# Kernel tuning notes

Hardware: AMD Instinct MI355X
Metric: run time of the kernel (lower is better)

The kernel has to match this reference:

```python
import jax, jax.numpy as jnp
import numpy as np

HEADS = 8

def _conv1x1(x, W, b):
    # x: [n, Cin, H, W]; W: [Cout, Cin]; b: [Cout]
    return jnp.einsum('nchw,oc->nohw', x, W) + b[None, :, None, None]

def setup_inputs() -> dict:
    key = jax.random.key(0)
    ks = jax.random.split(key, 11)
    n, Cin, H, W = 8, 256, 80, 80
    Ck, Cv = 256, 256
    s_in = 1.0 / np.sqrt(Cin)
    s_v = 1.0 / np.sqrt(Cv)
    return {
        'query_feature': jax.random.normal(ks[0], (n, Cin, H, W), jnp.float32),
        'key_feature': jax.random.normal(ks[1], (n, Cin, H, W), jnp.float32),
        'value_feature': jax.random.normal(ks[2], (n, Cin, H, W), jnp.float32),
        'Wq': jax.random.normal(ks[3], (Ck, Cin), jnp.float32) * s_in,
        'bq': jax.random.normal(ks[4], (Ck,), jnp.float32) * s_in,
        'Wk': jax.random.normal(ks[5], (Ck, Cin), jnp.float32) * s_in,
        'bk': jax.random.normal(ks[6], (Ck,), jnp.float32) * s_in,
        'Wv': jax.random.normal(ks[7], (Cv, Cin), jnp.float32) * s_in,
        'bv': jax.random.normal(ks[8], (Cv,), jnp.float32) * s_in,
        'Wr': jax.random.normal(ks[9], (Cin, Cv), jnp.float32) * s_v,
        'br': jax.random.normal(ks[10], (Cin,), jnp.float32) * s_v,
    }

def reference(query_feature, key_feature, value_feature, Wq, bq, Wk, bk, Wv, bv, Wr, br):
    n, _, qh, qw = query_feature.shape
    kvn, _, kvh, kvw = key_feature.shape
    Ck = Wq.shape[0]
    Cv = Wv.shape[0]
    hk = Ck // HEADS
    hv = Cv // HEADS
    Lq = qh * qw
    Lkv = kvh * kvw
    # 1x1 conv projections, split channels into heads (consecutive channel blocks)
    q = _conv1x1(query_feature, Wq, bq).reshape(n, HEADS, hk, Lq)
    k = _conv1x1(key_feature, Wk, bk).reshape(kvn, HEADS, hk, Lkv)
    v = _conv1x1(value_feature, Wv, bv).reshape(kvn, HEADS, hv, Lkv)
    # softmax: keys over spatial positions, queries over head channels
    k = jax.nn.softmax(k, axis=3)
    q = jax.nn.softmax(q, axis=2)
    # efficient (linear) attention: context = K @ V^T, out = context^T @ Q
    context = jnp.einsum('nhkl,nhvl->nhkv', k, v)          # [n, H, hk, hv]
    attended = jnp.einsum('nhkv,nhkl->nhvl', context, q)   # [n, H, hv, Lq]
    aggregated = attended.reshape(n, Cv, qh, qw)
    return _conv1x1(aggregated, Wr, br) + query_feature
```

## Files before the change

### kernel.cpp

```cpp
#include <hip/hip_runtime.h>
#include <hip/hip_bf16.h>

#define NB 8
#define C 256
#define LL 6400
#define HEADS 8
#define HC 32
#define NH 64
#define SEG 40
#define SL 160
#define ATP 40
#define QPP 264

typedef unsigned short u16;
typedef unsigned int u32;
typedef __attribute__((ext_vector_type(8))) short bf16x8;
typedef __attribute__((ext_vector_type(4))) float f32x4;

typedef __attribute__((address_space(1))) const u32 ga_u32;
typedef __attribute__((address_space(3))) u32 ls_u32;

__device__ __forceinline__ void gload_lds16(const u16* g, u16* l) {
  __builtin_amdgcn_global_load_lds((ga_u32*)g, (ls_u32*)l, 16, 0, 0);
}

__device__ __forceinline__ float bf2f(u32 u) { return __uint_as_float(u << 16); }
__device__ __forceinline__ u16 f2bf(float f) {
  __hip_bfloat16 h = __float2bfloat16(f);
  return *(u16*)&h;
}
__device__ __forceinline__ void unpack8(uint4 u, float* f) {
  f[0] = bf2f(u.x & 0xffffu); f[1] = bf2f(u.x >> 16);
  f[2] = bf2f(u.y & 0xffffu); f[3] = bf2f(u.y >> 16);
  f[4] = bf2f(u.z & 0xffffu); f[5] = bf2f(u.z >> 16);
  f[6] = bf2f(u.w & 0xffffu); f[7] = bf2f(u.w >> 16);
}

struct WcvtArgs { const float* W[3]; u16* Wb[3]; };
struct PFArgs { const float* X[3]; const u16* Wb[3]; const float* bias[3]; u16* P[3]; };

__global__ __launch_bounds__(256) void wcvt(WcvtArgs a) {
  const int idx = blockIdx.x * 256 + threadIdx.x;
  const int which = idx >> 14, off = (idx & 16383) * 4;
  float4 v = *(const float4*)&a.W[which][off];
  ushort4 o = {f2bf(v.x), f2bf(v.y), f2bf(v.z), f2bf(v.w)};
  *(ushort4*)&a.Wb[which][off] = o;
}

__global__ __launch_bounds__(256, 2) void proj_fused(PFArgs args) {
  __shared__ __align__(16) u16 At[128 * ATP];
  __shared__ __align__(16) u16 Bs[256 * 32];
  const int which = blockIdx.y >> 3, n = blockIdx.y & 7;
  const int l0 = blockIdx.x * 128;
  const int t = threadIdx.x;
  const int lane = t & 63, wave = t >> 6;
  const int fr = lane & 15, q = lane >> 4;
  const int wl = (wave >> 1) * 64, wco = (wave & 1) * 128;
  const int s32 = t & 31, rcg = t >> 5;
  const int srow = t >> 2, scol = (t & 3) * 8;
  const float* X = args.X[which] + (size_t)n * C * LL;
  const u16* Wb = args.Wb[which];
  f32x4 acc[4][8] = {};
  float4 xv[4];
#pragma unroll
  for (int j = 0; j < 4; ++j)
    xv[j] = *(const float4*)&X[(size_t)(rcg * 4 + j) * LL + l0 + s32 * 4];
  for (int k0 = 0; k0 < C; k0 += 32) {
    __syncthreads();
#pragma unroll
    for (int s = 0; s < 4; ++s)
      gload_lds16(&Wb[(size_t)(s * 64 + srow) * C + k0 + scol],
                  &Bs[s * 2048 + wave * 512]);
    const float* xf = (const float*)xv;
#pragma unroll
    for (int li = 0; li < 4; ++li) {
      const int lp = li ^ (s32 & 3);
      u32 lo = (u32)f2bf(xf[0 * 4 + lp]) | ((u32)f2bf(xf[1 * 4 + lp]) << 16);
      u32 hi = (u32)f2bf(xf[2 * 4 + lp]) | ((u32)f2bf(xf[3 * 4 + lp]) << 16);
      u32* dst = (u32*)&At[(s32 * 4 + lp) * ATP + rcg * 4];
      dst[0] = lo; dst[1] = hi;
    }
    __syncthreads();
    if (k0 + 32 < C) {
#pragma unroll
      for (int j = 0; j < 4; ++j)
        xv[j] = *(const float4*)&X[(size_t)(k0 + 32 + rcg * 4 + j) * LL + l0 + s32 * 4];
    }
    bf16x8 a[4];
#pragma unroll
    for (int i = 0; i < 4; ++i)
      a[i] = *(const bf16x8*)&At[(wl + i * 16 + fr) * ATP + q * 8];
#pragma unroll
    for (int j = 0; j < 8; ++j) {
      bf16x8 b = *(const bf16x8*)&Bs[(wco + j * 16 + fr) * 32 + q * 8];
#pragma unroll
      for (int i = 0; i < 4; ++i)
        acc[i][j] = __builtin_amdgcn_mfma_f32_16x16x32_bf16(a[i], b, acc[i][j], 0, 0, 0);
    }
  }
  const float* bias = args.bias[which];
  u16* P = args.P[which] + (size_t)n * LL * C;
  float bb[8];
#pragma unroll
  for (int j = 0; j < 8; ++j) bb[j] = bias[wco + j * 16 + fr];
#pragma unroll
  for (int i = 0; i < 4; ++i)
#pragma unroll
    for (int r = 0; r < 4; ++r) {
      const int lrow = l0 + wl + i * 16 + q * 4 + r;
#pragma unroll
      for (int j = 0; j < 8; ++j)
        P[(size_t)lrow * C + wco + j * 16 + fr] = f2bf(acc[i][j][r] + bb[j]);
    }
}

__global__ __launch_bounds__(256) void ctx_part(const u16* __restrict__ Kt,
    const u16* __restrict__ Vt, float* __restrict__ pctx, float* __restrict__ psum) {
  __shared__ __align__(16) u16 Ks[16 * 256];
  __shared__ __align__(16) u16 Vs[16 * 256];
  const int seg = blockIdx.x, n = blockIdx.y;
  const int t = threadIdx.x, lane = t & 63, wave = t >> 6;
  const int l0 = seg * SL;
  const u16* KtN = Kt + (size_t)n * LL * C;
  const u16* VtN = Vt + (size_t)n * LL * C;
  const int k4 = (lane & 7) * 4, v8 = lane >> 3;
  float acc[2][4][4] = {};
  float ssum[2][4] = {};
  for (int ls = 0; ls < SL; ls += 16) {
    __syncthreads();
#pragma unroll
    for (int i = 0; i < 2; ++i) {
      const int r = wave * 4 + i * 2;
      gload_lds16(&KtN[(size_t)(l0 + ls + r) * C + lane * 8], &Ks[r * 256]);
      gload_lds16(&VtN[(size_t)(l0 + ls + r) * C + lane * 8], &Vs[r * 256]);
    }
    __syncthreads();
#pragma unroll
    for (int hh = 0; hh < 2; ++hh) {
      const int h = wave * 2 + hh;
#pragma unroll
      for (int l = 0; l < 16; ++l) {
        ushort4 ku = *(const ushort4*)&Ks[l * 256 + h * 32 + k4];
        ushort4 vu = *(const ushort4*)&Vs[l * 256 + h * 32 + v8 * 4];
        float ek[4] = {__expf(bf2f(ku.x)), __expf(bf2f(ku.y)),
                       __expf(bf2f(ku.z)), __expf(bf2f(ku.w))};
        float vf[4] = {bf2f(vu.x), bf2f(vu.y), bf2f(vu.z), bf2f(vu.w)};
#pragma unroll
        for (int i = 0; i < 4; ++i)
#pragma unroll
          for (int j = 0; j < 4; ++j) acc[hh][i][j] = fmaf(ek[i], vf[j], acc[hh][i][j]);
        if (v8 == 0)
#pragma unroll
          for (int i = 0; i < 4; ++i) ssum[hh][i] += ek[i];
      }
    }
  }
#pragma unroll
  for (int hh = 0; hh < 2; ++hh) {
    const int h = wave * 2 + hh;
    const size_t pb = ((size_t)seg * NH + n * 8 + h) * 1024;
#pragma unroll
    for (int i = 0; i < 4; ++i)
#pragma unroll
      for (int j = 0; j < 4; ++j)
        pctx[pb + (size_t)(k4 + i) * 32 + v8 * 4 + j] = acc[hh][i][j];
    if (v8 == 0) {
      const size_t sb = ((size_t)seg * NH + n * 8 + h) * 32;
#pragma unroll
      for (int i = 0; i < 4; ++i) psum[sb + k4 + i] = ssum[hh][i];
    }
  }
}

__global__ __launch_bounds__(256) void ctx_reduce(const float* __restrict__ pctx,
    const float* __restrict__ psum, float* __restrict__ ctx) {
  const int idx = blockIdx.x * 256 + threadIdx.x;
  const int nh = idx >> 10, e = idx & 1023, k = e >> 5;
  float s = 0.f, ss = 0.f;
  for (int g = 0; g < SEG; ++g) {
    s += pctx[(size_t)(g * NH + nh) * 1024 + e];
    ss += psum[(size_t)(g * NH + nh) * 32 + k];
  }
  ctx[idx] = s / ss;
}

__global__ __launch_bounds__(256) void mfuse(const float* __restrict__ Wr,
    const float* __restrict__ ctx, u16* __restrict__ M) {
  const int idx = blockIdx.x * 256 + threadIdx.x;
  const int hk = idx & 255;
  const int o = (idx >> 8) & 255;
  const int n = idx >> 16;
  const int h = hk >> 5, k = hk & 31;
  const float* wr = Wr + (size_t)o * C + h * HC;
  const float* cx = ctx + ((size_t)(n * HEADS + h) * HC + k) * HC;
  float s = 0.f;
#pragma unroll
  for (int v = 0; v < HC; ++v) s = fmaf(wr[v], cx[v], s);
  M[idx] = f2bf(s);
}

__global__ __launch_bounds__(256) void out_fused(const u16* __restrict__ Qt,
    const u16* __restrict__ Mb, const float* __restrict__ br,
    const float* __restrict__ Xq, float* __restrict__ out) {
  __shared__ __align__(16) u16 Qp[64 * QPP];
  __shared__ __align__(16) u16 As[128 * 32];
  const int n = blockIdx.y, l0 = blockIdx.x * 64;
  const int t = threadIdx.x, lane = t & 63, wave = t >> 6;
  const int fr = lane & 15, q = lane >> 4;
  const int wcoL = (wave >> 1) * 64, wl = (wave & 1) * 32;
  const u16* QtN = Qt + (size_t)n * LL * C;
#pragma unroll
  for (int p = 0; p < 2; ++p) {
    const int row = p * 32 + (t >> 3);
    const int g = t & 7;
    const uint4* src = (const uint4*)&QtN[(size_t)(l0 + row) * C + g * 32];
    uint4 u0 = src[0], u1 = src[1], u2 = src[2], u3 = src[3];
    float v[32];
    unpack8(u0, v); unpack8(u1, v + 8); unpack8(u2, v + 16); unpack8(u3, v + 24);
    float e[32], s = 0.f;
#pragma unroll
    for (int j = 0; j < 32; ++j) { e[j] = __expf(v[j]); s += e[j]; }
    const float r = 1.0f / s;
    uint4* drow = (uint4*)&Qp[row * QPP + g * 32];
#pragma unroll
    for (int b4 = 0; b4 < 4; ++b4) {
      union { uint4 u; u16 h[8]; } o;
#pragma unroll
      for (int j = 0; j < 8; ++j) o.h[j] = f2bf(e[b4 * 8 + j] * r);
      drow[b4] = o.u;
    }
  }
  f32x4 acc[2][4][2] = {};
  const u16* MbN = Mb + (size_t)n * C * C;
  const int srow = t >> 2, scol = (t & 3) * 8;
  for (int coh = 0; coh < 2; ++coh)
    for (int k0 = 0; k0 < C; k0 += 32) {
      __syncthreads();
#pragma unroll
      for (int s = 0; s < 2; ++s)
        gload_lds16(&MbN[(size_t)(coh * 128 + s * 64 + srow) * C + k0 + scol],
                    &As[s * 2048 + wave * 512]);
      __syncthreads();
      bf16x8 a[4], b[2];
#pragma unroll
      for (int i = 0; i < 4; ++i)
        a[i] = *(const bf16x8*)&As[(wcoL + i * 16 + fr) * 32 + q * 8];
#pragma unroll
      for (int j = 0; j < 2; ++j)
        b[j] = *(const bf16x8*)&Qp[(wl + j * 16 + fr) * QPP + k0 + q * 8];
#pragma unroll
      for (int i = 0; i < 4; ++i)
#pragma unroll
        for (int j = 0; j < 2; ++j)
          acc[coh][i][j] = __builtin_amdgcn_mfma_f32_16x16x32_bf16(a[i], b[j], acc[coh][i][j], 0, 0, 0);
    }
  const float* XqN = Xq + (size_t)n * C * LL;
  float* On = out + (size_t)n * C * LL;
#pragma unroll
  for (int coh = 0; coh < 2; ++coh)
#pragma unroll
    for (int i = 0; i < 4; ++i)
#pragma unroll
      for (int r = 0; r < 4; ++r) {
        const int co = coh * 128 + wcoL + i * 16 + q * 4 + r;
        const float bb = br[co];
#pragma unroll
        for (int j = 0; j < 2; ++j) {
          const int l = l0 + wl + j * 16 + fr;
          const size_t off = (size_t)co * LL + l;
          On[off] = acc[coh][i][j][r] + bb + XqN[off];
        }
      }
}

extern "C" void kernel_launch(void* const* d_in, const int* in_sizes, int n_in,
                              void* d_out, int out_size, void* d_ws, size_t ws_size,
                              hipStream_t stream) {
  const float* Xq = (const float*)d_in[0];
  const float* Xk = (const float*)d_in[1];
  const float* Xv = (const float*)d_in[2];
  const float* Wq = (const float*)d_in[3];
  const float* bq = (const float*)d_in[4];
  const float* Wk = (const float*)d_in[5];
  const float* bk = (const float*)d_in[6];
  const float* Wv = (const float*)d_in[7];
  const float* bv = (const float*)d_in[8];
  const float* Wr = (const float*)d_in[9];
  const float* br = (const float*)d_in[10];
  float* out = (float*)d_out;

  char* ws = (char*)d_ws;
  const size_t nelem = (size_t)NB * LL * C;
  u16* Qt = (u16*)ws;
  u16* Kt = (u16*)(ws + nelem * 2);
  u16* Vt = (u16*)(ws + nelem * 4);
  char* p = ws + nelem * 6;
  u16* Wqb = (u16*)p; p += C * C * 2;
  u16* Wkb = (u16*)p; p += C * C * 2;
  u16* Wvb = (u16*)p; p += C * C * 2;
  float* pctx = (float*)p; p += (size_t)SEG * NH * HC * HC * 4;
  float* psum = (float*)p; p += (size_t)SEG * NH * HC * 4;
  float* ctx = (float*)p;  p += (size_t)NH * HC * HC * 4;
  u16* Mb = (u16*)p;

  WcvtArgs wa;
  wa.W[0] = Wq; wa.W[1] = Wk; wa.W[2] = Wv;
  wa.Wb[0] = Wqb; wa.Wb[1] = Wkb; wa.Wb[2] = Wvb;
  wcvt<<<192, 256, 0, stream>>>(wa);

  PFArgs pa;
  pa.X[0] = Xq; pa.X[1] = Xk; pa.X[2] = Xv;
  pa.Wb[0] = Wqb; pa.Wb[1] = Wkb; pa.Wb[2] = Wvb;
  pa.bias[0] = bq; pa.bias[1] = bk; pa.bias[2] = bv;
  pa.P[0] = Qt; pa.P[1] = Kt; pa.P[2] = Vt;
  proj_fused<<<dim3(50, 24), 256, 0, stream>>>(pa);

  ctx_part<<<dim3(SEG, NB), 256, 0, stream>>>(Kt, Vt, pctx, psum);
  ctx_reduce<<<NH * HC * HC / 256, 256, 0, stream>>>(pctx, psum, ctx);
  mfuse<<<NB * C * C / 256, 256, 0, stream>>>(Wr, ctx, Mb);
  out_fused<<<dim3(100, NB), 256, 0, stream>>>(Qt, Mb, br, Xq, out);
}
```

Baseline: 347.5 us.

## Double-buffer LDS tiles in projection and output GEMM kernels

Converts the K-loops of proj_fused and out_fused to use double-buffered LDS tiles. The next tile's weight/M loads and X conversion are issued before the current tile's MFMAs, with one barrier per iteration instead of two and explicit waitcnt/sched_barrier control. This is meant to overlap global-to-LDS transfers with compute. In exchange it doubles LDS use, which may reduce occupancy, and relies on hand-tuned vmcnt counts that must match the number of outstanding loads.

```diff
diff --git a/kernel.cpp b/kernel.cpp
--- a/kernel.cpp
+++ b/kernel.cpp
@@ -48,8 +48,8 @@
 }
 
 __global__ __launch_bounds__(256, 2) void proj_fused(PFArgs args) {
-  __shared__ __align__(16) u16 At[128 * ATP];
-  __shared__ __align__(16) u16 Bs[256 * 32];
+  __shared__ __align__(16) u16 At[2][128 * ATP];
+  __shared__ __align__(16) u16 Bs[2][256 * 32];
   const int which = blockIdx.y >> 3, n = blockIdx.y & 7;
   const int l0 = blockIdx.x * 128;
   const int t = threadIdx.x;
@@ -62,42 +62,81 @@
   const u16* Wb = args.Wb[which];
   f32x4 acc[4][8] = {};
   float4 xv[4];
+
 #pragma unroll
   for (int j = 0; j < 4; ++j)
     xv[j] = *(const float4*)&X[(size_t)(rcg * 4 + j) * LL + l0 + s32 * 4];
-  for (int k0 = 0; k0 < C; k0 += 32) {
-    __syncthreads();
-#pragma unroll
-    for (int s = 0; s < 4; ++s)
-      gload_lds16(&Wb[(size_t)(s * 64 + srow) * C + k0 + scol],
-                  &Bs[s * 2048 + wave * 512]);
+#pragma unroll
+  for (int s = 0; s < 4; ++s)
+    gload_lds16(&Wb[(size_t)(s * 64 + srow) * C + scol], &Bs[0][s * 2048 + wave * 512]);
+  {
     const float* xf = (const float*)xv;
 #pragma unroll
     for (int li = 0; li < 4; ++li) {
       const int lp = li ^ (s32 & 3);
       u32 lo = (u32)f2bf(xf[0 * 4 + lp]) | ((u32)f2bf(xf[1 * 4 + lp]) << 16);
       u32 hi = (u32)f2bf(xf[2 * 4 + lp]) | ((u32)f2bf(xf[3 * 4 + lp]) << 16);
-      u32* dst = (u32*)&At[(s32 * 4 + lp) * ATP + rcg * 4];
+      u32* dst = (u32*)&At[0][(s32 * 4 + lp) * ATP + rcg * 4];
       dst[0] = lo; dst[1] = hi;
     }
-    __syncthreads();
-    if (k0 + 32 < C) {
-#pragma unroll
-      for (int j = 0; j < 4; ++j)
-        xv[j] = *(const float4*)&X[(size_t)(k0 + 32 + rcg * 4 + j) * LL + l0 + s32 * 4];
+  }
+  __builtin_amdgcn_sched_barrier(0);
+#pragma unroll
+  for (int j = 0; j < 4; ++j)
+    xv[j] = *(const float4*)&X[(size_t)(32 + rcg * 4 + j) * LL + l0 + s32 * 4];
+  asm volatile("s_waitcnt vmcnt(4) lgkmcnt(0)" ::: "memory");
+  __builtin_amdgcn_s_barrier();
+  __builtin_amdgcn_sched_barrier(0);
+
+#pragma unroll
+  for (int kt = 0; kt < 8; ++kt) {
+    u16* Atc = At[kt & 1];
+    u16* Bsc = Bs[kt & 1];
+    if (kt < 7) {
+      u16* Atn = At[(kt & 1) ^ 1];
+      u16* Bsn = Bs[(kt & 1) ^ 1];
+#pragma unroll
+      for (int s = 0; s < 4; ++s)
+        gload_lds16(&Wb[(size_t)(s * 64 + srow) * C + (kt + 1) * 32 + scol],
+                    &Bsn[s * 2048 + wave * 512]);
+      const float* xf = (const float*)xv;
+#pragma unroll
+      for (int li = 0; li < 4; ++li) {
+        const int lp = li ^ (s32 & 3);
+        u32 lo = (u32)f2bf(xf[0 * 4 + lp]) | ((u32)f2bf(xf[1 * 4 + lp]) << 16);
+        u32 hi = (u32)f2bf(xf[2 * 4 + lp]) | ((u32)f2bf(xf[3 * 4 + lp]) << 16);
+        u32* dst = (u32*)&Atn[(s32 * 4 + lp) * ATP + rcg * 4];
+        dst[0] = lo; dst[1] = hi;
+      }
+      __builtin_amdgcn_sched_barrier(0);
+      if (kt < 6) {
+#pragma unroll
+        for (int j = 0; j < 4; ++j)
+          xv[j] = *(const float4*)&X[(size_t)((kt + 2) * 32 + rcg * 4 + j) * LL + l0 + s32 * 4];
+      }
     }
     bf16x8 a[4];
 #pragma unroll
     for (int i = 0; i < 4; ++i)
-      a[i] = *(const bf16x8*)&At[(wl + i * 16 + fr) * ATP + q * 8];
+      a[i] = *(const bf16x8*)&Atc[(wl + i * 16 + fr) * ATP + q * 8];
 #pragma unroll
     for (int j = 0; j < 8; ++j) {
-      bf16x8 b = *(const bf16x8*)&Bs[(wco + j * 16 + fr) * 32 + q * 8];
+      bf16x8 b = *(const bf16x8*)&Bsc[(wco + j * 16 + fr) * 32 + q * 8];
 #pragma unroll
       for (int i = 0; i < 4; ++i)
         acc[i][j] = __builtin_amdgcn_mfma_f32_16x16x32_bf16(a[i], b, acc[i][j], 0, 0, 0);
     }
-  }
+    if (kt < 6) {
+      asm volatile("s_waitcnt vmcnt(4) lgkmcnt(0)" ::: "memory");
+      __builtin_amdgcn_s_barrier();
+      __builtin_amdgcn_sched_barrier(0);
+    } else if (kt == 6) {
+      asm volatile("s_waitcnt vmcnt(0) lgkmcnt(0)" ::: "memory");
+      __builtin_amdgcn_s_barrier();
+      __builtin_amdgcn_sched_barrier(0);
+    }
+  }
+
   const float* bias = args.bias[which];
   u16* P = args.P[which] + (size_t)n * LL * C;
   float bb[8];
@@ -203,12 +242,19 @@
     const u16* __restrict__ Mb, const float* __restrict__ br,
     const float* __restrict__ Xq, float* __restrict__ out) {
   __shared__ __align__(16) u16 Qp[64 * QPP];
-  __shared__ __align__(16) u16 As[128 * 32];
+  __shared__ __align__(16) u16 As[2][128 * 32];
   const int n = blockIdx.y, l0 = blockIdx.x * 64;
   const int t = threadIdx.x, lane = t & 63, wave = t >> 6;
   const int fr = lane & 15, q = lane >> 4;
   const int wcoL = (wave >> 1) * 64, wl = (wave & 1) * 32;
+  const int srow = t >> 2, scol = (t & 3) * 8;
   const u16* QtN = Qt + (size_t)n * LL * C;
+  const u16* MbN = Mb + (size_t)n * C * C;
+
+#pragma unroll
+  for (int s = 0; s < 2; ++s)
+    gload_lds16(&MbN[(size_t)(s * 64 + srow) * C + scol], &As[0][s * 2048 + wave * 512]);
+
 #pragma unroll
   for (int p = 0; p < 2; ++p) {
     const int row = p * 32 + (t >> 3);
@@ -230,30 +276,41 @@
       drow[b4] = o.u;
     }
   }
+  asm volatile("s_waitcnt vmcnt(0) lgkmcnt(0)" ::: "memory");
+  __builtin_amdgcn_s_barrier();
+  __builtin_amdgcn_sched_barrier(0);
+
   f32x4 acc[2][4][2] = {};
-  const u16* MbN = Mb + (size_t)n * C * C;
-  const int srow = t >> 2, scol = (t & 3) * 8;
-  for (int coh = 0; coh < 2; ++coh)
-    for (int k0 = 0; k0 < C; k0 += 32) {
-      __syncthreads();
+#pragma unroll
+  for (int it = 0; it < 16; ++it) {
+    const int coh = it >> 3, k0 = (it & 7) * 32, cur = it & 1;
+    if (it < 15) {
+      const int nco = (it + 1) >> 3, nk0 = ((it + 1) & 7) * 32;
 #pragma unroll
       for (int s = 0; s < 2; ++s)
-        gload_lds16(&MbN[(size_t)(coh * 128 + s * 64 + srow) * C + k0 + scol],
-                    &As[s * 2048 + wave * 512]);
-      __syncthreads();
-      bf16x8 a[4], b[2];
-#pragma unroll
-      for (int i = 0; i < 4; ++i)
-        a[i] = *(const bf16x8*)&As[(wcoL + i * 16 + fr) * 32 + q * 8];
+        gload_lds16(&MbN[(size_t)(nco * 128 + s * 64 + srow) * C + nk0 + scol],
+                    &As[cur ^ 1][s * 2048 + wave * 512]);
+      __builtin_amdgcn_sched_barrier(0);
+    }
+    bf16x8 a[4], b[2];
+#pragma unroll
+    for (int i = 0; i < 4; ++i)
+      a[i] = *(const bf16x8*)&As[cur][(wcoL + i * 16 + fr) * 32 + q * 8];
+#pragma unroll
+    for (int j = 0; j < 2; ++j)
+      b[j] = *(const bf16x8*)&Qp[(wl + j * 16 + fr) * QPP + k0 + q * 8];
+#pragma unroll
+    for (int i = 0; i < 4; ++i)
 #pragma unroll
       for (int j = 0; j < 2; ++j)
-        b[j] = *(const bf16x8*)&Qp[(wl + j * 16 + fr) * QPP + k0 + q * 8];
-#pragma unroll
-      for (int i = 0; i < 4; ++i)
-#pragma unroll
-        for (int j = 0; j < 2; ++j)
-          acc[coh][i][j] = __builtin_amdgcn_mfma_f32_16x16x32_bf16(a[i], b[j], acc[coh][i][j], 0, 0, 0);
-    }
+        acc[coh][i][j] = __builtin_amdgcn_mfma_f32_16x16x32_bf16(a[i], b[j], acc[coh][i][j], 0, 0, 0);
+    if (it < 15) {
+      asm volatile("s_waitcnt vmcnt(0) lgkmcnt(0)" ::: "memory");
+      __builtin_amdgcn_s_barrier();
+      __builtin_amdgcn_sched_barrier(0);
+    }
+  }
+
   const float* XqN = Xq + (size_t)n * C * LL;
   float* On = out + (size_t)n * C * LL;
 #pragma unroll
```

After: 344.6 us. Within noise of the previous version (-0.8%).
